# Kernel optimization log

Hardware: AMD Instinct MI355X
Metric: run time of the kernel (lower is better)

Reference implementation:

```python
import jax, jax.numpy as jnp
import numpy as np

B, S, D, H, DK, DFF = 4, 2048, 512, 8, 64, 2048
MAX_DIST = 2047  # effective_dist = min(MAX_DIST, S-1) = S-1, required by the skew reshape
EPS = 1e-6


def setup_inputs() -> dict:
    key = jax.random.key(0)
    ks = jax.random.split(key, 12)
    w = lambda k, shape: jax.random.normal(k, shape, jnp.float32) * 0.02
    return {
        "x": jax.random.normal(ks[0], (B, S, D), jnp.float32),
        "mask": jnp.tril(jnp.ones((1, 1, S, S), jnp.int32)),  # causal
        "wq": w(ks[1], (D, D)),
        "wk": w(ks[2], (D, D)),
        "wv": w(ks[3], (D, D)),
        "w0": w(ks[4], (D, D)),
        "b0": jnp.zeros((D,), jnp.float32),
        "rel_emb": w(ks[5], (H, MAX_DIST + 1, DK)),
        "ln1_g": jnp.ones((D,), jnp.float32),
        "ln1_b": jnp.zeros((D,), jnp.float32),
        "ln2_g": jnp.ones((D,), jnp.float32),
        "ln2_b": jnp.zeros((D,), jnp.float32),
        "ff_w1": w(ks[6], (D, DFF)),
        "ff_b1": jnp.zeros((DFF,), jnp.float32),
        "ff_w2": w(ks[7], (DFF, D)),
        "ff_b2": jnp.zeros((D,), jnp.float32),
    }


def _layernorm(t, g, b):
    mu = t.mean(-1, keepdims=True)
    var = ((t - mu) ** 2).mean(-1, keepdims=True)
    return (t - mu) * jax.lax.rsqrt(var + EPS) * g + b


def _rel_scores(q, rel_emb):
    # q: [B,H,S,DK]; rel_emb: [H, MAX_DIST+1, DK]
    eff = min(MAX_DIST, S - 1)                      # static
    q_er = jnp.einsum('bhid,hrd->bhir', q, rel_emb[:, :eff + 1])  # [B,H,S,S]
    padded = jnp.pad(q_er, ((0, 0), (0, 0), (0, 0), (1, 0)))      # [B,H,S,S+1]
    # skew trick: reinterpret and drop first row -> [B,H,S,S]
    return padded.reshape(B, H, S + 1, S)[:, :, 1:, :]


def reference(x, mask, wq, wk, wv, w0, b0, rel_emb,
              ln1_g, ln1_b, ln2_g, ln2_b, ff_w1, ff_b1, ff_w2, ff_b2):
    scale = float(np.sqrt(DK))
    # --- self-attention sublayer (pre-norm residual) ---
    h = _layernorm(x, ln1_g, ln1_b)
    q = (h @ wq).reshape(B, S, H, DK).transpose(0, 2, 1, 3)  # [B,H,S,DK]
    k = (h @ wk).reshape(B, S, H, DK).transpose(0, 2, 1, 3)
    v = (h @ wv).reshape(B, S, H, DK).transpose(0, 2, 1, 3)
    content = jnp.einsum('bhid,bhjd->bhij', q, k) / scale     # [B,H,S,S]
    scores = content + _rel_scores(q, rel_emb)
    scores = jnp.where(mask == 0, jnp.float32(-1e9), scores)
    probs = jax.nn.softmax(scores, axis=-1)
    attn = jnp.einsum('bhij,bhjd->bhid', probs, v)            # [B,H,S,DK]
    attn = attn.transpose(0, 2, 1, 3).reshape(B, S, D)
    x = x + (attn @ w0 + b0)
    # --- feed-forward sublayer (pre-norm residual) ---
    h2 = _layernorm(x, ln2_g, ln2_b)
    ff = jax.nn.relu(h2 @ ff_w1 + ff_b1) @ ff_w2 + ff_b2
    return x + ff
```

## Files before the change

### kernel.cpp

```cpp
#include <hip/hip_runtime.h>
#include <hip/hip_bf16.h>

#define SB 2048
#define DB 512
#define HB 8
#define DKB 64
#define DFB 2048
#define BATCH 4
#define BSTR 92

typedef __attribute__((ext_vector_type(8))) short bf16x8;
typedef __attribute__((ext_vector_type(4))) float f32x4;
typedef __attribute__((ext_vector_type(2))) float f32x2;
typedef __attribute__((ext_vector_type(2))) unsigned u32x2;
typedef __attribute__((ext_vector_type(4))) short s16x4;

static __device__ __forceinline__ short f2bf(float x) {
  union { float f; unsigned u; } v; v.f = x;
  unsigned r = (v.u + 0x7fffu + ((v.u >> 16) & 1u)) >> 16;
  return (short)(unsigned short)r;
}

static __device__ __forceinline__ float bflo(unsigned u) {
  union { unsigned x; float f; } v; v.x = u << 16; return v.f;
}
static __device__ __forceinline__ float bfhi(unsigned u) {
  union { unsigned x; float f; } v; v.x = u & 0xffff0000u; return v.f;
}

static __device__ __forceinline__ unsigned pack2bf(float a, float b) {
  return (unsigned)(unsigned short)f2bf(a) | ((unsigned)(unsigned short)f2bf(b) << 16);
}

static __device__ __forceinline__ f32x4 mfma16(bf16x8 a, bf16x8 b, f32x4 c) {
  return __builtin_amdgcn_mfma_f32_16x16x32_bf16(a, b, c, 0, 0, 0);
}

static __device__ __forceinline__ void gload_lds16(const short* g, short* l) {
  __builtin_amdgcn_global_load_lds(
      (const __attribute__((address_space(1))) unsigned*)g,
      (__attribute__((address_space(3))) unsigned*)l, 16, 0, 0);
}

__global__ __launch_bounds__(256) void conv_kernel(const float* __restrict__ src,
                                                   short* __restrict__ dst, int n) {
  int i = blockIdx.x * 256 + threadIdx.x;
  if (i < n) dst[i] = f2bf(src[i]);
}

__global__ __launch_bounds__(256) void tconv_kernel(const float* __restrict__ src,
                                                    short* __restrict__ dst,
                                                    int K, int N, float scale) {
  __shared__ float t[64][65];
  int n0 = blockIdx.x * 64, k0 = blockIdx.y * 64;
  int cn = threadIdx.x & 63, rk = threadIdx.x >> 6;
#pragma unroll
  for (int r = 0; r < 16; ++r)
    t[rk + r * 4][cn] = src[(size_t)(k0 + rk + r * 4) * N + n0 + cn];
  __syncthreads();
#pragma unroll
  for (int r = 0; r < 16; ++r)
    dst[(size_t)(n0 + rk + r * 4) * K + k0 + cn] = f2bf(t[cn][rk + r * 4] * scale);
}

__global__ __launch_bounds__(256) void tconv4_kernel(
    const float* __restrict__ s0, const float* __restrict__ s1,
    const float* __restrict__ s2, const float* __restrict__ s3,
    short* __restrict__ dst) {
  __shared__ float t[64][65];
  int z = blockIdx.z;
  const float* src = z == 0 ? s0 : (z == 1 ? s1 : (z == 2 ? s2 : s3));
  float scale = (z == 1) ? 0.125f : 1.f;
  short* d = dst + (size_t)z * 512 * 512;
  int n0 = blockIdx.x * 64, k0 = blockIdx.y * 64;
  int cn = threadIdx.x & 63, rk = threadIdx.x >> 6;
#pragma unroll
  for (int r = 0; r < 16; ++r)
    t[rk + r * 4][cn] = src[(size_t)(k0 + rk + r * 4) * 512 + n0 + cn];
  __syncthreads();
#pragma unroll
  for (int r = 0; r < 16; ++r)
    d[(size_t)(n0 + rk + r * 4) * 512 + k0 + cn] = f2bf(t[cn][rk + r * 4] * scale);
}

__global__ __launch_bounds__(256) void ln_kernel(const float* __restrict__ in,
                                                 const float* __restrict__ g,
                                                 const float* __restrict__ bb,
                                                 short* __restrict__ out) {
  int w = threadIdx.x >> 6, l = threadIdx.x & 63;
  size_t row = (size_t)blockIdx.x * 4 + w;
  const float* xr = in + row * DB;
  f32x4 v0 = *(const f32x4*)(xr + l * 8);
  f32x4 v1 = *(const f32x4*)(xr + l * 8 + 4);
  float s = (v0[0] + v0[1]) + (v0[2] + v0[3]) + (v1[0] + v1[1]) + (v1[2] + v1[3]);
  float s2 = (v0[0] * v0[0] + v0[1] * v0[1]) + (v0[2] * v0[2] + v0[3] * v0[3]) +
             (v1[0] * v1[0] + v1[1] * v1[1]) + (v1[2] * v1[2] + v1[3] * v1[3]);
#pragma unroll
  for (int off = 1; off < 64; off <<= 1) {
    s += __shfl_xor(s, off, 64);
    s2 += __shfl_xor(s2, off, 64);
  }
  float mean = s * (1.f / DB);
  float var = s2 * (1.f / DB) - mean * mean;
  float rstd = rsqrtf(var + 1e-6f);
  f32x4 g0 = *(const f32x4*)(g + l * 8);
  f32x4 g1 = *(const f32x4*)(g + l * 8 + 4);
  f32x4 b0 = *(const f32x4*)(bb + l * 8);
  f32x4 b1 = *(const f32x4*)(bb + l * 8 + 4);
  bf16x8 ov;
#pragma unroll
  for (int e = 0; e < 4; ++e) ov[e] = f2bf((v0[e] - mean) * rstd * g0[e] + b0[e]);
#pragma unroll
  for (int e = 0; e < 4; ++e) ov[4 + e] = f2bf((v1[e] - mean) * rstd * g1[e] + b1[e]);
  *(bf16x8*)(out + row * DB + l * 8) = ov;
}

template <int KD, int EPI>
__global__ __launch_bounds__(256) void gemm_kernel(
    const short* __restrict__ A, const short* __restrict__ BT,
    const float* __restrict__ bias, const float* __restrict__ resid,
    short* __restrict__ o0, short* __restrict__ o1, short* __restrict__ o2,
    float* __restrict__ of) {
  __shared__ short As[2][4096];
  __shared__ short Bs[2][4096];
  int tid = threadIdx.x;
  int l = tid & 63, w = tid >> 6;
  int wr = w >> 1, wc = w & 1;
  int lr = l & 15, lq = l >> 4;
  int row0 = blockIdx.y * 128;
  int col0 = blockIdx.x * 128;

  f32x4 acc[4][4];
#pragma unroll
  for (int a = 0; a < 4; ++a)
#pragma unroll
    for (int b = 0; b < 4; ++b) acc[a][b] = (f32x4){0.f, 0.f, 0.f, 0.f};

  const short* gA = A + (size_t)(row0 + (tid >> 2)) * KD + (tid & 3) * 8;
  const short* gB = BT + (size_t)(col0 + (tid >> 2)) * KD + (tid & 3) * 8;
  const size_t step64 = (size_t)64 * KD;
  int woff = w * 512;

  auto stage = [&](int buf, int k0) {
    gload_lds16(gA + k0, As[buf] + woff);
    gload_lds16(gA + step64 + k0, As[buf] + woff + 2048);
    gload_lds16(gB + k0, Bs[buf] + woff);
    gload_lds16(gB + step64 + k0, Bs[buf] + woff + 2048);
  };

  stage(0, 0);
  __syncthreads();
  int cur = 0;
  for (int k0 = 0; k0 < KD; k0 += 32) {
    if (k0 + 32 < KD) stage(cur ^ 1, k0 + 32);
    bf16x8 af[4], bfv[4];
#pragma unroll
    for (int a = 0; a < 4; ++a)
      af[a] = *(const bf16x8*)(As[cur] + (wr * 64 + a * 16 + lr) * 32 + lq * 8);
#pragma unroll
    for (int b = 0; b < 4; ++b)
      bfv[b] = *(const bf16x8*)(Bs[cur] + (wc * 64 + b * 16 + lr) * 32 + lq * 8);
#pragma unroll
    for (int a = 0; a < 4; ++a)
#pragma unroll
      for (int b = 0; b < 4; ++b)
        acc[a][b] = mfma16(af[a], bfv[b], acc[a][b]);
    __syncthreads();
    cur ^= 1;
  }

#pragma unroll
  for (int a = 0; a < 4; ++a)
#pragma unroll
    for (int b = 0; b < 4; ++b) {
      size_t colb = (size_t)col0 + wc * 64 + b * 16 + lr;
      if (EPI == 0 && (int)(colb >> 9) == 2) {
        int d = (int)(colb & 63);
        size_t rowb = (size_t)row0 + wr * 64 + a * 16 + lq * 4;
        size_t b_ = rowb >> 11, s_ = rowb & 2047;
        size_t bh = b_ * HB + (int)((colb >> 6) & 7);
        s16x4 pkv;
#pragma unroll
        for (int r = 0; r < 4; ++r) pkv[r] = f2bf(acc[a][b][r]);
        *(s16x4*)(o2 + (bh * DKB + d) * SB + s_) = pkv;
        continue;
      }
#pragma unroll
      for (int r = 0; r < 4; ++r) {
        size_t row = (size_t)row0 + wr * 64 + a * 16 + lq * 4 + r;
        size_t col = colb;
        float val = acc[a][b][r];
        if (EPI == 0) {
          int sect = (int)(col >> 9);
          int hh = (int)((col >> 6) & 7);
          int d = (int)(col & 63);
          size_t b_ = row >> 11, s_ = row & 2047;
          size_t bh = b_ * HB + hh;
          short bv = f2bf(val);
          if (sect == 0) o0[(bh * SB + s_) * DKB + d] = bv;
          else o1[(bh * SB + s_) * DKB + d] = bv;
        } else if (EPI == 1) {
          of[row * DB + col] = resid[row * DB + col] + val + bias[col];
        } else {
          float tv = val + bias[col];
          o0[row * DFB + col] = f2bf(tv > 0.f ? tv : 0.f);
        }
      }
    }
}

template <int KD>
__global__ __launch_bounds__(256) void gemm64_kernel(
    const short* __restrict__ A, const short* __restrict__ BT,
    const float* __restrict__ bias, const float* __restrict__ resid,
    float* __restrict__ of) {
  __shared__ short As[2][4096];
  __shared__ short Bs[2][2048];
  int tid = threadIdx.x;
  int l = tid & 63, w = tid >> 6;
  int lr = l & 15, lq = l >> 4;
  int row0 = blockIdx.y * 128;
  int col0 = blockIdx.x * 64;

  f32x4 acc[2][4];
#pragma unroll
  for (int a = 0; a < 2; ++a)
#pragma unroll
    for (int b = 0; b < 4; ++b) acc[a][b] = (f32x4){0.f, 0.f, 0.f, 0.f};

  const short* gA = A + (size_t)(row0 + (tid >> 2)) * KD + (tid & 3) * 8;
  const short* gB = BT + (size_t)(col0 + (tid >> 2)) * KD + (tid & 3) * 8;
  const size_t step64 = (size_t)64 * KD;
  int woff = w * 512;

  auto stage = [&](int buf, int k0) {
    gload_lds16(gA + k0, As[buf] + woff);
    gload_lds16(gA + step64 + k0, As[buf] + woff + 2048);
    gload_lds16(gB + k0, Bs[buf] + woff);
  };

  stage(0, 0);
  __syncthreads();
  int cur = 0;
  for (int k0 = 0; k0 < KD; k0 += 32) {
    if (k0 + 32 < KD) stage(cur ^ 1, k0 + 32);
    bf16x8 af[2], bfv[4];
#pragma unroll
    for (int a = 0; a < 2; ++a)
      af[a] = *(const bf16x8*)(As[cur] + (w * 32 + a * 16 + lr) * 32 + lq * 8);
#pragma unroll
    for (int b = 0; b < 4; ++b)
      bfv[b] = *(const bf16x8*)(Bs[cur] + (b * 16 + lr) * 32 + lq * 8);
#pragma unroll
    for (int a = 0; a < 2; ++a)
#pragma unroll
      for (int b = 0; b < 4; ++b)
        acc[a][b] = mfma16(af[a], bfv[b], acc[a][b]);
    __syncthreads();
    cur ^= 1;
  }

#pragma unroll
  for (int a = 0; a < 2; ++a)
#pragma unroll
    for (int b = 0; b < 4; ++b)
#pragma unroll
      for (int r = 0; r < 4; ++r) {
        size_t row = (size_t)row0 + w * 32 + a * 16 + lq * 4 + r;
        size_t col = (size_t)col0 + b * 16 + lr;
        of[row * DB + col] = resid[row * DB + col] + acc[a][b][r] + bias[col];
      }
}

static __device__ __forceinline__ void e_phase_lds(const short* Ebuf, int w, int ph,
                                                   bf16x8 q0, bf16x8 q1,
                                                   short* bdx, int lr, int lq) {
  bf16x8 ef[10];
#pragma unroll
  for (int nt = 0; nt < 5; ++nt) {
    int re = 48 - 16 * w + nt * 16 + lr;
    int sr = (re + ph) & 127;
    const short* eb = Ebuf + sr * 64;
    ef[nt * 2] = *(const bf16x8*)(eb + ((lq ^ (sr & 7)) << 3));
    ef[nt * 2 + 1] = *(const bf16x8*)(eb + (((lq + 4) ^ (sr & 7)) << 3));
  }
  const f32x4 zz = {0.f, 0.f, 0.f, 0.f};
#pragma unroll
  for (int nt = 0; nt < 5; ++nt) {
    f32x4 rr = mfma16(ef[nt * 2 + 1], q1, mfma16(ef[nt * 2], q0, zz));
    u32x2 pk = {pack2bf(rr[0], rr[1]), pack2bf(rr[2], rr[3])};
    *(u32x2*)((char*)bdx + lr * (BSTR * 2) + (nt * 16 + lq * 4) * 2) = pk;
  }
}

static __device__ __forceinline__ void sm_step(const f32x4* sc, const short* bd,
                                               short* pb, f32x4* acc,
                                               float& mrun, float& lsum,
                                               int i0, int j0, int lr, int lq) {
  int bbase = lq * 4 + 15 - lr;
  int o = bbase & 3;
  unsigned shb = (unsigned)(o & 1) * 16;
  bool hi2 = (o >= 2);
  float bv[4][4];
#pragma unroll
  for (int hh = 0; hh < 4; ++hh) {
    int w0 = (hh * 16 + bbase) & ~3;
    const unsigned* p = (const unsigned*)(bd + lr * BSTR + w0);
    unsigned W0 = p[0], W1 = p[1], W2 = p[2], W3 = p[3];
    unsigned X0 = hi2 ? W1 : W0;
    unsigned X1 = hi2 ? W2 : W1;
    unsigned X2 = hi2 ? W3 : W2;
    unsigned out0 = (unsigned)((((unsigned long long)X1 << 32) | X0) >> shb);
    unsigned out1 = (unsigned)((((unsigned long long)X2 << 32) | X1) >> shb);
    bv[hh][0] = bflo(out0);
    bv[hh][1] = bfhi(out0);
    bv[hh][2] = bflo(out1);
    bv[hh][3] = bfhi(out1);
  }
  float s[4][4];
  if (j0 + 63 > i0) {
    int thr = i0 + lr - j0;
#pragma unroll
    for (int hh = 0; hh < 4; ++hh)
#pragma unroll
      for (int r = 0; r < 4; ++r) {
        int n = hh * 16 + lq * 4 + r;
        float v = sc[hh][r] + bv[hh][r];
        s[hh][r] = (n <= thr) ? v : -1e30f;
      }
  } else {
#pragma unroll
    for (int hh = 0; hh < 4; ++hh)
#pragma unroll
      for (int r = 0; r < 4; ++r) s[hh][r] = sc[hh][r] + bv[hh][r];
  }
  float m0 = fmaxf(fmaxf(s[0][0], s[0][1]), fmaxf(s[0][2], s[0][3]));
  float m1 = fmaxf(fmaxf(s[1][0], s[1][1]), fmaxf(s[1][2], s[1][3]));
  float m2 = fmaxf(fmaxf(s[2][0], s[2][1]), fmaxf(s[2][2], s[2][3]));
  float m3 = fmaxf(fmaxf(s[3][0], s[3][1]), fmaxf(s[3][2], s[3][3]));
  float tm = fmaxf(fmaxf(m0, m1), fmaxf(m2, m3));
  if (!__all(tm <= mrun + 8.f)) {
    float tr = fmaxf(tm, __shfl_xor(tm, 16, 64));
    tr = fmaxf(tr, __shfl_xor(tr, 32, 64));
    float mnew = fmaxf(mrun, tr);
    float corr = __expf(mrun - mnew);
    mrun = mnew;
    lsum *= corr;
#pragma unroll
    for (int dt = 0; dt < 4; ++dt) acc[dt] *= corr;
  }
#pragma unroll
  for (int hh = 0; hh < 4; ++hh) {
    float p0 = __expf(s[hh][0] - mrun);
    float p1 = __expf(s[hh][1] - mrun);
    float p2 = __expf(s[hh][2] - mrun);
    float p3 = __expf(s[hh][3] - mrun);
    lsum += (p0 + p1) + (p2 + p3);
    u32x2 pk = {pack2bf(p0, p1), pack2bf(p2, p3)};
    int byteoff = lr * (BSTR * 2) + ((((hh << 1) | (lq >> 1)) ^ (lr & 7)) << 4) + ((lq & 1) << 3);
    *(u32x2*)((char*)pb + byteoff) = pk;
  }
}

static __device__ __forceinline__ void pv_step(const short* pb, const bf16x8* vf,
                                               f32x4* acc, int lr, int lq) {
#pragma unroll
  for (int kc = 0; kc < 2; ++kc) {
    bf16x8 pf = *(const bf16x8*)((const char*)pb + lr * (BSTR * 2) +
                                 ((((kc << 2) | lq) ^ (lr & 7)) << 4));
    __builtin_amdgcn_s_setprio(1);
#pragma unroll
    for (int dt = 0; dt < 4; ++dt)
      acc[dt] = mfma16(vf[kc * 4 + dt], pf, acc[dt]);
    __builtin_amdgcn_s_setprio(0);
  }
}

static __device__ __forceinline__ void attn_out(const f32x4* acc, float lsum,
                                                short* out, int bh, int i0,
                                                int lr, int lq) {
  float lt = lsum + __shfl_xor(lsum, 16, 64);
  lt += __shfl_xor(lt, 32, 64);
  float inv = 1.f / lt;
  int b_ = bh >> 3, hd = bh & 7;
  short* orow = out + ((size_t)(b_ * SB + i0 + lr) * DB + hd * 64);
#pragma unroll
  for (int dt = 0; dt < 4; ++dt) {
    s16x4 pkv;
#pragma unroll
    for (int r = 0; r < 4; ++r) pkv[r] = f2bf(acc[dt][r] * inv);
    *(s16x4*)(orow + dt * 16 + lq * 4) = pkv;
  }
}

__global__ __launch_bounds__(256, 2) void attn_kernel(
    const short* __restrict__ Q, const short* __restrict__ Kb,
    const short* __restrict__ VT, const short* __restrict__ Eb,
    short* __restrict__ out) {
  __shared__ short Ks[4096];
  __shared__ short Vs[4096];
  __shared__ short Elo_s[8192];
  __shared__ short Ehi_s[8192];
  __shared__ short bandP[4][2][16][BSTR];
  int tid = threadIdx.x;
  int l = tid & 63, w = tid >> 6;
  int lr = l & 15, lq = l >> 4;
  int bid = blockIdx.x;
  int s = bid >> 3;
  int bh = (bid & 7) * 4 + (s >> 4);
  int g = s & 15;
  int qb0 = g << 6;
  int qb1 = (31 - g) << 6;
  int i0lo = qb0 + (w << 4);
  int i0hi = qb1 + (w << 4);
  const short* Qh = Q + (size_t)bh * SB * DKB;
  const short* Kh = Kb + (size_t)bh * SB * DKB;
  const short* Vh = VT + (size_t)bh * DKB * SB;
  const short* Eh = Eb + (size_t)(bh & 7) * SB * DKB;

  bf16x8 ql0 = *(const bf16x8*)(Qh + (size_t)(i0lo + lr) * DKB + lq * 8);
  bf16x8 ql1 = *(const bf16x8*)(Qh + (size_t)(i0lo + lr) * DKB + 32 + lq * 8);
  bf16x8 qh0 = *(const bf16x8*)(Qh + (size_t)(i0hi + lr) * DKB + lq * 8);
  bf16x8 qh1 = *(const bf16x8*)(Qh + (size_t)(i0hi + lr) * DKB + 32 + lq * 8);

  int lrow = l >> 3, lch = l & 7;
  int rKV = (w << 4) + lrow;
  int cKV = lch ^ (rKV & 7);
  int cE = lch ^ lrow;

  const f32x4 zz = {0.f, 0.f, 0.f, 0.f};
  f32x4 accL[4], accH[4];
#pragma unroll
  for (int dt = 0; dt < 4; ++dt) { accL[dt] = zz; accH[dt] = zz; }
  float mL = -1e30f, lsL = 0.f, mH = -1e30f, lsH = 0.f;
  short* bdL = &bandP[w][0][0][0];
  short* bdH = &bandP[w][1][0][0];

  for (int j0 = 0; j0 < qb1 + 64; j0 += 64) {
    gload_lds16(Kh + (size_t)(j0 + rKV) * DKB + cKV * 8, Ks + (w << 10));
    gload_lds16(Kh + (size_t)(j0 + rKV + 8) * DKB + cKV * 8, Ks + (w << 10) + 512);
    gload_lds16(Vh + (size_t)rKV * SB + j0 + cKV * 8, Vs + (w << 10));
    gload_lds16(Vh + (size_t)(rKV + 8) * SB + j0 + cKV * 8, Vs + (w << 10) + 512);
    int rbHi = SB - 64 - qb1 + j0;
    int phHi = rbHi & 64;
    if (j0 == 0) {
#pragma unroll
      for (int ii = 0; ii < 4; ++ii) {
        int rr = (w << 5) + lrow + ii * 8;
        int er = rbHi + rr;
        er = er < SB ? er : SB - 1;
        int slot0 = ((w << 5) + ii * 8 + phHi) & 127;
        gload_lds16(Eh + (size_t)er * DKB + cE * 8, Ehi_s + (slot0 << 6));
      }
    } else {
#pragma unroll
      for (int ii = 0; ii < 2; ++ii) {
        int rr = (w << 4) + lrow + ii * 8;
        int er = rbHi + 64 + rr;
        er = er < SB ? er : SB - 1;
        int slot0 = ((w << 4) + ii * 8 + (phHi ^ 64)) & 127;
        gload_lds16(Eh + (size_t)er * DKB + cE * 8, Ehi_s + (slot0 << 6));
      }
    }
    int rbLo = SB - 64 - qb0 + j0;
    int phLo = rbLo & 64;
    if (j0 <= qb0 + 63) {
      if (j0 == 0) {
#pragma unroll
        for (int ii = 0; ii < 4; ++ii) {
          int rr = (w << 5) + lrow + ii * 8;
          int er = rbLo + rr;
          er = er < SB ? er : SB - 1;
          int slot0 = ((w << 5) + ii * 8 + phLo) & 127;
          gload_lds16(Eh + (size_t)er * DKB + cE * 8, Elo_s + (slot0 << 6));
        }
      } else {
#pragma unroll
        for (int ii = 0; ii < 2; ++ii) {
          int rr = (w << 4) + lrow + ii * 8;
          int er = rbLo + 64 + rr;
          er = er < SB ? er : SB - 1;
          int slot0 = ((w << 4) + ii * 8 + (phLo ^ 64)) & 127;
          gload_lds16(Eh + (size_t)er * DKB + cE * 8, Elo_s + (slot0 << 6));
        }
      }
    }
    __syncthreads();
    bool actLo = (j0 <= i0lo + 15);
    {
      bf16x8 kf[8];
#pragma unroll
      for (int hh = 0; hh < 4; ++hh) {
        int rk = hh * 16 + lr;
        const short* kb = Ks + rk * 64;
        kf[hh * 2] = *(const bf16x8*)(kb + ((lq ^ (rk & 7)) << 3));
        kf[hh * 2 + 1] = *(const bf16x8*)(kb + (((lq + 4) ^ (rk & 7)) << 3));
      }
      f32x4 scH[4], scL[4];
#pragma unroll
      for (int hh = 0; hh < 4; ++hh)
        scH[hh] = mfma16(kf[hh * 2 + 1], qh1, mfma16(kf[hh * 2], qh0, zz));
      if (actLo) {
#pragma unroll
        for (int hh = 0; hh < 4; ++hh)
          scL[hh] = mfma16(kf[hh * 2 + 1], ql1, mfma16(kf[hh * 2], ql0, zz));
      }
      bf16x8 vf[8];
#pragma unroll
      for (int kc = 0; kc < 2; ++kc)
#pragma unroll
        for (int dt = 0; dt < 4; ++dt) {
          int rv = dt * 16 + lr;
          vf[kc * 4 + dt] = *(const bf16x8*)(Vs + rv * 64 +
                                             (((kc * 4 + lq) ^ (rv & 7)) << 3));
        }
      e_phase_lds(Ehi_s, w, phHi, qh0, qh1, bdH, lr, lq);
      if (actLo) e_phase_lds(Elo_s, w, phLo, ql0, ql1, bdL, lr, lq);
      sm_step(scH, bdH, bdH, accH, mH, lsH, i0hi, j0, lr, lq);
      if (actLo) sm_step(scL, bdL, bdL, accL, mL, lsL, i0lo, j0, lr, lq);
      pv_step(bdH, vf, accH, lr, lq);
      if (actLo) pv_step(bdL, vf, accL, lr, lq);
    }
    __syncthreads();
  }
  attn_out(accH, lsH, out, bh, i0hi, lr, lq);
  attn_out(accL, lsL, out, bh, i0lo, lr, lq);
}

extern "C" void kernel_launch(void* const* d_in, const int* in_sizes, int n_in,
                              void* d_out, int out_size, void* d_ws, size_t ws_size,
                              hipStream_t stream) {
  const float* x    = (const float*)d_in[0];
  const float* wq   = (const float*)d_in[2];
  const float* wk   = (const float*)d_in[3];
  const float* wv   = (const float*)d_in[4];
  const float* w0   = (const float*)d_in[5];
  const float* b0   = (const float*)d_in[6];
  const float* rel  = (const float*)d_in[7];
  const float* ln1g = (const float*)d_in[8];
  const float* ln1b = (const float*)d_in[9];
  const float* ln2g = (const float*)d_in[10];
  const float* ln2b = (const float*)d_in[11];
  const float* fw1  = (const float*)d_in[12];
  const float* fb1  = (const float*)d_in[13];
  const float* fw2  = (const float*)d_in[14];
  const float* fb2  = (const float*)d_in[15];
  float* outp = (float*)d_out;

  char* ws = (char*)d_ws;
  size_t off = 0;
  auto alloc = [&](size_t bytes) {
    char* p = ws + off;
    off += (bytes + 255) & ~(size_t)255;
    return p;
  };
  short* wqkvT = (short*)alloc((size_t)1536 * 512 * 2);
  short* w0T   = (short*)alloc((size_t)512 * 512 * 2);
  short* fw1T  = (short*)alloc((size_t)2048 * 512 * 2);
  short* fw2T  = (short*)alloc((size_t)512 * 2048 * 2);
  short* relb  = (short*)alloc((size_t)8 * 2048 * 64 * 2);
  short* hbuf  = (short*)alloc((size_t)8192 * 512 * 2);
  short* Qb    = (short*)alloc((size_t)8192 * 512 * 2);
  short* Kbf   = (short*)alloc((size_t)8192 * 512 * 2);
  short* VTb   = (short*)alloc((size_t)8192 * 512 * 2);
  short* attnb = (short*)alloc((size_t)8192 * 512 * 2);
  float* x2    = (float*)alloc((size_t)8192 * 512 * 4);
  short* ff1 = hbuf;
  short* h2  = attnb;
  (void)w0T;

  dim3 blk(256);
  conv_kernel<<<(8 * 2048 * 64 + 255) / 256, blk, 0, stream>>>(rel, relb, 8 * 2048 * 64);
  tconv4_kernel<<<dim3(8, 8, 4), blk, 0, stream>>>(wq, wk, wv, w0, wqkvT);
  tconv_kernel<<<dim3(32, 8), blk, 0, stream>>>(fw1, fw1T, 512, 2048, 1.f);
  tconv_kernel<<<dim3(8, 32), blk, 0, stream>>>(fw2, fw2T, 2048, 512, 1.f);

  ln_kernel<<<2048, blk, 0, stream>>>(x, ln1g, ln1b, hbuf);
  gemm_kernel<512, 0><<<dim3(12, 64), blk, 0, stream>>>(hbuf, wqkvT, nullptr, nullptr,
                                                        Qb, Kbf, VTb, nullptr);
  attn_kernel<<<512, blk, 0, stream>>>(Qb, Kbf, VTb, relb, attnb);
  gemm64_kernel<512><<<dim3(8, 64), blk, 0, stream>>>(attnb, wqkvT + (size_t)3 * 512 * 512,
                                                      b0, x, x2);
  ln_kernel<<<2048, blk, 0, stream>>>(x2, ln2g, ln2b, h2);
  gemm_kernel<512, 2><<<dim3(16, 64), blk, 0, stream>>>(h2, fw1T, fb1, nullptr,
                                                        ff1, nullptr, nullptr, nullptr);
  gemm64_kernel<2048><<<dim3(8, 64), blk, 0, stream>>>(ff1, fw2T, fb2, x2, outp);
}
```

Baseline: 226.8 us.

## Double GEMM K-tile with XOR-swizzled LDS and use exp2 softmax via folded log2e

The two GEMM kernels now stage K in 64-wide tiles instead of 32-wide ones. The LDS rows use an XOR swizzle on both the global-to-LDS copy and the fragment reads, which halves the number of barrier-separated iterations and is meant to avoid bank conflicts. Separately, log2(e) is folded into the Q weight conversion so the attention softmax can use exp2f directly, saving a multiply per exponential. The cost is doubled LDS per GEMM block, which may lower occupancy, plus bf16 rounding of the rescaled Q weights.

```diff
diff --git a/kernel.cpp b/kernel.cpp
--- a/kernel.cpp
+++ b/kernel.cpp
@@ -70,7 +70,7 @@
   __shared__ float t[64][65];
   int z = blockIdx.z;
   const float* src = z == 0 ? s0 : (z == 1 ? s1 : (z == 2 ? s2 : s3));
-  float scale = (z == 1) ? 0.125f : 1.f;
+  float scale = (z == 0) ? 1.4426950408889634f : ((z == 1) ? 0.125f : 1.f);
   short* d = dst + (size_t)z * 512 * 512;
   int n0 = blockIdx.x * 64, k0 = blockIdx.y * 64;
   int cn = threadIdx.x & 63, rk = threadIdx.x >> 6;
@@ -121,8 +121,8 @@
     const float* __restrict__ bias, const float* __restrict__ resid,
     short* __restrict__ o0, short* __restrict__ o1, short* __restrict__ o2,
     float* __restrict__ of) {
-  __shared__ short As[2][4096];
-  __shared__ short Bs[2][4096];
+  __shared__ short As[2][8192];
+  __shared__ short Bs[2][8192];
   int tid = threadIdx.x;
   int l = tid & 63, w = tid >> 6;
   int wr = w >> 1, wc = w & 1;
@@ -136,35 +136,43 @@
 #pragma unroll
     for (int b = 0; b < 4; ++b) acc[a][b] = (f32x4){0.f, 0.f, 0.f, 0.f};
 
-  const short* gA = A + (size_t)(row0 + (tid >> 2)) * KD + (tid & 3) * 8;
-  const short* gB = BT + (size_t)(col0 + (tid >> 2)) * KD + (tid & 3) * 8;
-  const size_t step64 = (size_t)64 * KD;
-  int woff = w * 512;
+  int srow = tid >> 3;
+  int scol = (tid & 7) ^ (srow & 7);
+  const short* gA = A + (size_t)(row0 + srow) * KD + scol * 8;
+  const short* gB = BT + (size_t)(col0 + srow) * KD + scol * 8;
 
   auto stage = [&](int buf, int k0) {
-    gload_lds16(gA + k0, As[buf] + woff);
-    gload_lds16(gA + step64 + k0, As[buf] + woff + 2048);
-    gload_lds16(gB + k0, Bs[buf] + woff);
-    gload_lds16(gB + step64 + k0, Bs[buf] + woff + 2048);
+#pragma unroll
+    for (int ro = 0; ro < 4; ++ro) {
+      gload_lds16(gA + (size_t)(ro * 32) * KD + k0, As[buf] + ro * 2048 + w * 512);
+      gload_lds16(gB + (size_t)(ro * 32) * KD + k0, Bs[buf] + ro * 2048 + w * 512);
+    }
   };
 
   stage(0, 0);
   __syncthreads();
   int cur = 0;
-  for (int k0 = 0; k0 < KD; k0 += 32) {
-    if (k0 + 32 < KD) stage(cur ^ 1, k0 + 32);
-    bf16x8 af[4], bfv[4];
-#pragma unroll
-    for (int a = 0; a < 4; ++a)
-      af[a] = *(const bf16x8*)(As[cur] + (wr * 64 + a * 16 + lr) * 32 + lq * 8);
-#pragma unroll
-    for (int b = 0; b < 4; ++b)
-      bfv[b] = *(const bf16x8*)(Bs[cur] + (wc * 64 + b * 16 + lr) * 32 + lq * 8);
-#pragma unroll
-    for (int a = 0; a < 4; ++a)
-#pragma unroll
-      for (int b = 0; b < 4; ++b)
-        acc[a][b] = mfma16(af[a], bfv[b], acc[a][b]);
+  for (int k0 = 0; k0 < KD; k0 += 64) {
+    if (k0 + 64 < KD) stage(cur ^ 1, k0 + 64);
+#pragma unroll
+    for (int kk = 0; kk < 2; ++kk) {
+      bf16x8 af[4], bfv[4];
+#pragma unroll
+      for (int a = 0; a < 4; ++a) {
+        int rk = wr * 64 + a * 16 + lr;
+        af[a] = *(const bf16x8*)(As[cur] + rk * 64 + ((((kk << 2) | lq) ^ (rk & 7)) << 3));
+      }
+#pragma unroll
+      for (int b = 0; b < 4; ++b) {
+        int rk = wc * 64 + b * 16 + lr;
+        bfv[b] = *(const bf16x8*)(Bs[cur] + rk * 64 + ((((kk << 2) | lq) ^ (rk & 7)) << 3));
+      }
+#pragma unroll
+      for (int a = 0; a < 4; ++a)
+#pragma unroll
+        for (int b = 0; b < 4; ++b)
+          acc[a][b] = mfma16(af[a], bfv[b], acc[a][b]);
+    }
     __syncthreads();
     cur ^= 1;
   }
@@ -214,8 +222,8 @@
     const short* __restrict__ A, const short* __restrict__ BT,
     const float* __restrict__ bias, const float* __restrict__ resid,
     float* __restrict__ of) {
-  __shared__ short As[2][4096];
-  __shared__ short Bs[2][2048];
+  __shared__ short As[2][8192];
+  __shared__ short Bs[2][4096];
   int tid = threadIdx.x;
   int l = tid & 63, w = tid >> 6;
   int lr = l & 15, lq = l >> 4;
@@ -228,34 +236,44 @@
 #pragma unroll
     for (int b = 0; b < 4; ++b) acc[a][b] = (f32x4){0.f, 0.f, 0.f, 0.f};
 
-  const short* gA = A + (size_t)(row0 + (tid >> 2)) * KD + (tid & 3) * 8;
-  const short* gB = BT + (size_t)(col0 + (tid >> 2)) * KD + (tid & 3) * 8;
-  const size_t step64 = (size_t)64 * KD;
-  int woff = w * 512;
+  int srow = tid >> 3;
+  int scol = (tid & 7) ^ (srow & 7);
+  const short* gA = A + (size_t)(row0 + srow) * KD + scol * 8;
+  const short* gB = BT + (size_t)(col0 + srow) * KD + scol * 8;
 
   auto stage = [&](int buf, int k0) {
-    gload_lds16(gA + k0, As[buf] + woff);
-    gload_lds16(gA + step64 + k0, As[buf] + woff + 2048);
-    gload_lds16(gB + k0, Bs[buf] + woff);
+#pragma unroll
+    for (int ro = 0; ro < 4; ++ro)
+      gload_lds16(gA + (size_t)(ro * 32) * KD + k0, As[buf] + ro * 2048 + w * 512);
+#pragma unroll
+    for (int ro = 0; ro < 2; ++ro)
+      gload_lds16(gB + (size_t)(ro * 32) * KD + k0, Bs[buf] + ro * 2048 + w * 512);
   };
 
   stage(0, 0);
   __syncthreads();
   int cur = 0;
-  for (int k0 = 0; k0 < KD; k0 += 32) {
-    if (k0 + 32 < KD) stage(cur ^ 1, k0 + 32);
-    bf16x8 af[2], bfv[4];
-#pragma unroll
-    for (int a = 0; a < 2; ++a)
-      af[a] = *(const bf16x8*)(As[cur] + (w * 32 + a * 16 + lr) * 32 + lq * 8);
-#pragma unroll
-    for (int b = 0; b < 4; ++b)
-      bfv[b] = *(const bf16x8*)(Bs[cur] + (b * 16 + lr) * 32 + lq * 8);
-#pragma unroll
-    for (int a = 0; a < 2; ++a)
-#pragma unroll
-      for (int b = 0; b < 4; ++b)
-        acc[a][b] = mfma16(af[a], bfv[b], acc[a][b]);
+  for (int k0 = 0; k0 < KD; k0 += 64) {
+    if (k0 + 64 < KD) stage(cur ^ 1, k0 + 64);
+#pragma unroll
+    for (int kk = 0; kk < 2; ++kk) {
+      bf16x8 af[2], bfv[4];
+#pragma unroll
+      for (int a = 0; a < 2; ++a) {
+        int rk = w * 32 + a * 16 + lr;
+        af[a] = *(const bf16x8*)(As[cur] + rk * 64 + ((((kk << 2) | lq) ^ (rk & 7)) << 3));
+      }
+#pragma unroll
+      for (int b = 0; b < 4; ++b) {
+        int rk = b * 16 + lr;
+        bfv[b] = *(const bf16x8*)(Bs[cur] + rk * 64 + ((((kk << 2) | lq) ^ (rk & 7)) << 3));
+      }
+#pragma unroll
+      for (int a = 0; a < 2; ++a)
+#pragma unroll
+        for (int b = 0; b < 4; ++b)
+          acc[a][b] = mfma16(af[a], bfv[b], acc[a][b]);
+    }
     __syncthreads();
     cur ^= 1;
   }
@@ -343,7 +361,7 @@
     float tr = fmaxf(tm, __shfl_xor(tm, 16, 64));
     tr = fmaxf(tr, __shfl_xor(tr, 32, 64));
     float mnew = fmaxf(mrun, tr);
-    float corr = __expf(mrun - mnew);
+    float corr = exp2f(mrun - mnew);
     mrun = mnew;
     lsum *= corr;
 #pragma unroll
@@ -351,10 +369,10 @@
   }
 #pragma unroll
   for (int hh = 0; hh < 4; ++hh) {
-    float p0 = __expf(s[hh][0] - mrun);
-    float p1 = __expf(s[hh][1] - mrun);
-    float p2 = __expf(s[hh][2] - mrun);
-    float p3 = __expf(s[hh][3] - mrun);
+    float p0 = exp2f(s[hh][0] - mrun);
+    float p1 = exp2f(s[hh][1] - mrun);
+    float p2 = exp2f(s[hh][2] - mrun);
+    float p3 = exp2f(s[hh][3] - mrun);
     lsum += (p0 + p1) + (p2 + p3);
     u32x2 pk = {pack2bf(p0, p1), pack2bf(p2, p3)};
     int byteoff = lr * (BSTR * 2) + ((((hh << 1) | (lq >> 1)) ^ (lr & 7)) << 4) + ((lq & 1) << 3);
```

Measured after the change: 232.1 us. +2.4%, slower.
